# Kernel optimization log

Hardware: AMD Instinct MI355X
Metric: run time of the kernel (lower is better)

The kernel has to match this reference:

```python
import jax, jax.numpy as jnp
import numpy as np
import math
from jax import lax

TAU = 2
SIGMA_D2 = (TAU / 1.5) ** 2
SIGMA_TH2 = math.radians(20.0) ** 2

_offs = range(-TAU, TAU + 1)
OFFSETS = np.array([(dz, dy, dx) for dz in _offs for dy in _offs for dx in _offs
                    if dz or dy or dx], dtype=np.int32)  # (124, 3)
W_DIST = np.exp(-(OFFSETS.astype(np.float64) ** 2).sum(1) / SIGMA_D2).astype(np.float32)


def setup_inputs() -> dict:
    key = jax.random.key(0)
    k1, k2 = jax.random.split(key)
    n_pred = jax.random.normal(k1, (2, 3, 64, 64, 64), dtype=jnp.float32)
    source_pred = jax.random.normal(k2, (2, 1, 64, 64, 64), dtype=jnp.float32)
    return {"n_pred": n_pred, "source_pred": source_pred}


def reference(n_pred, source_pred):
    B, C, D, H, W = n_pred.shape
    pad = TAU
    # F.normalize(p=2, dim=1, eps=1e-6): divide by max(norm, eps)
    norm = jnp.sqrt(jnp.sum(n_pred * n_pred, axis=1, keepdims=True))
    n = n_pred / jnp.maximum(norm, 1e-6)

    prob = jax.nn.sigmoid(source_pred)            # (B,1,D,H,W)
    central_mask = prob > 0.5                      # (B,1,D,H,W)

    spat = ((0, 0), (0, 0), (pad, pad), (pad, pad), (pad, pad))
    padded_n = jnp.pad(n, spat)                    # zero pad like F.pad value=0
    padded_p = jnp.pad(prob, spat)

    offsets = jnp.asarray(OFFSETS)                 # (124,3)
    w_dist = jnp.asarray(W_DIST, dtype=n.dtype)    # (124,)

    def body(carry, xs):
        off, wd = xs
        start_n = (0, 0, pad + off[0], pad + off[1], pad + off[2])
        shifted_n = lax.dynamic_slice(padded_n, start_n, (B, C, D, H, W))
        shifted_p = lax.dynamic_slice(padded_p, start_n, (B, 1, D, H, W))
        dot = jnp.clip(jnp.sum(n * shifted_n, axis=1), -1.0, 1.0)  # (B,D,H,W)
        theta2 = jnp.arccos(dot) ** 2
        w_theta = jnp.exp(-theta2 / SIGMA_TH2)
        m = (central_mask & (shifted_p > 0.5))[:, 0].astype(n.dtype)  # (B,D,H,W)
        total, count = carry
        total = total + wd * jnp.sum(w_theta * m)
        count = count + jnp.sum(m)
        return (total, count), None

    init = (jnp.zeros((), n.dtype), jnp.zeros((), n.dtype))
    (total, count), _ = lax.scan(body, init, (offsets, w_dist))
    # reduction='mean' over masked elements; 0 if no valid pairs
    return jnp.where(count == 0, jnp.zeros((), n.dtype), total / count)
```

## Files before the change

### kernel.cpp

```cpp
#include <hip/hip_runtime.h>
#include <math.h>

#define PD 68
#define PD2 (PD * PD)
#define PVOL (PD * PD * PD)
#define NBLK2 2048

#define KE (-16.4140429822f)


__global__ __launch_bounds__(256) void pad_normalize_kernel(
    const float* __restrict__ n_pred,
    const float* __restrict__ src,
    float4* __restrict__ q)
{
    int idx = blockIdx.x * 256 + threadIdx.x;
    if (idx >= 2 * PVOL) return;
    int b = idx / PVOL;
    int r = idx - b * PVOL;
    int z = r / PD2;
    int r2 = r - z * PD2;
    int y = r2 / PD;
    int x = r2 - y * PD;
    int gx = x - 2, gy = y - 2, gz = z - 2;
    float4 v = make_float4(0.f, 0.f, 0.f, 0.f);
    if ((unsigned)gx < 64u && (unsigned)gy < 64u && (unsigned)gz < 64u) {
        const size_t cs = 262144;
        size_t vox = ((size_t)gz * 64 + gy) * 64 + gx;
        size_t off = (size_t)b * 3 * cs + vox;
        float xx = n_pred[off];
        float yy = n_pred[off + cs];
        float zz = n_pred[off + 2 * cs];
        float inv = 1.0f / fmaxf(sqrtf(xx * xx + yy * yy + zz * zz), 1e-6f);
        float m = (src[(size_t)b * cs + vox] > 0.0f) ? 1.0f : 0.0f;
        v = make_float4(xx * inv, yy * inv, zz * inv, m);
    }
    q[idx] = v;
}


__global__ __launch_bounds__(256) void stencil_kernel(
    const float4* __restrict__ q, float2* __restrict__ partials)
{
    int x = threadIdx.x & 63;
    int y = blockIdx.x * 4 + (threadIdx.x >> 6);
    int z = blockIdx.y;
    int b = blockIdx.z;
    const float4* cp =
        q + (size_t)b * PVOL + ((size_t)(z + 2) * PD + (y + 2)) * PD + (x + 2);
    float4 c = cp[0];
    float tot = 0.0f, cf = 0.0f;
    if (c.w != 0.0f) {
#pragma unroll
        for (int dz = 0; dz <= 2; ++dz) {
#pragma unroll
            for (int dy = -2; dy <= 2; ++dy) {
#pragma unroll
                for (int dx = -2; dx <= 2; ++dx) {
                    if (dz == 0 && dy < 0) continue;
                    if (dz == 0 && dy == 0 && dx <= 0) continue;
                    const float coff =
                        -0.5625f * (float)(dz * dz + dy * dy + dx * dx);
                    float4 nb = cp[(dz * PD + dy) * PD + dx];
                    float dot = fmaf(c.x, nb.x, fmaf(c.y, nb.y, c.z * nb.z));
                    float u = 1.0f - dot;
                    float p = fmaf(u, 1.8990885e-3f, 5.5803571e-3f);
                    p = fmaf(u, p, 1.8750000e-2f);
                    p = fmaf(u, p, 8.3333333e-2f);
                    p = fmaf(u, p, 1.0f);
                    float uh = u * p * p;
                    float w = __expf(fmaf(KE, uh, coff));
                    tot = fmaf(w, nb.w, tot);
                    cf += nb.w;
                }
            }
        }
    }
#pragma unroll
    for (int s = 32; s > 0; s >>= 1) {
        tot += __shfl_down(tot, s, 64);
        cf  += __shfl_down(cf, s, 64);
    }
    __shared__ float sd[4], sc[4];
    int wid = threadIdx.x >> 6, lane = threadIdx.x & 63;
    if (lane == 0) { sd[wid] = tot; sc[wid] = cf; }
    __syncthreads();
    if (threadIdx.x == 0) {
        int bid = ((int)blockIdx.z * gridDim.y + blockIdx.y) * gridDim.x
                  + blockIdx.x;
        partials[bid] = make_float2(sd[0] + sd[1] + sd[2] + sd[3],
                                    sc[0] + sc[1] + sc[2] + sc[3]);
    }
}

__global__ __launch_bounds__(256) void reduce_kernel(
    const float2* __restrict__ partials, float* __restrict__ out)
{
    double t = 0.0, c = 0.0;
    for (int i = threadIdx.x; i < NBLK2; i += 256) {
        float2 p = partials[i];
        t += (double)p.x;
        c += (double)p.y;
    }
#pragma unroll
    for (int s = 32; s > 0; s >>= 1) {
        t += __shfl_down(t, s, 64);
        c += __shfl_down(c, s, 64);
    }
    __shared__ double sd[4], sc[4];
    int wid = threadIdx.x >> 6, lane = threadIdx.x & 63;
    if (lane == 0) { sd[wid] = t; sc[wid] = c; }
    __syncthreads();
    if (threadIdx.x == 0) {
        double T = sd[0] + sd[1] + sd[2] + sd[3];
        double C = sc[0] + sc[1] + sc[2] + sc[3];
        out[0] = (C == 0.0) ? 0.0f : (float)(T / C);
    }
}


#define TILE 8
#define HALO 2
#define LDIM 12
#define LSZ  1728
#define NVOX 512

__global__ __launch_bounds__(256) void repulsion_fused_kernel(
    const float* __restrict__ n_pred, const float* __restrict__ src,
    double* __restrict__ acc)
{
    __shared__ float4 sn[LSZ];
    __shared__ float rd[4], rc[4];
    const int tx = blockIdx.x * TILE, ty = blockIdx.y * TILE;
    const int b = blockIdx.z >> 3, tz = (blockIdx.z & 7) * TILE;
    const size_t cs = 262144;
    const float* npb = n_pred + (size_t)b * 3 * cs;
    const float* spb = src + (size_t)b * cs;
    for (int i = threadIdx.x; i < LSZ; i += 256) {
        int lx = i % LDIM, t = i / LDIM, ly = t % LDIM, lz = t / LDIM;
        int gx = tx + lx - HALO, gy = ty + ly - HALO, gz = tz + lz - HALO;
        float4 v = make_float4(0.f, 0.f, 0.f, 0.f);
        if ((unsigned)gx < 64u && (unsigned)gy < 64u && (unsigned)gz < 64u) {
            size_t off = ((size_t)gz * 64 + gy) * 64 + gx;
            float x = npb[off], y = npb[cs + off], z = npb[2 * cs + off];
            float inv = 1.0f / fmaxf(sqrtf(x * x + y * y + z * z), 1e-6f);
            float m = (spb[off] > 0.0f) ? 1.0f : 0.0f;
            v = make_float4(x * inv, y * inv, z * inv, m);
        }
        sn[i] = v;
    }
    __syncthreads();
    float tot = 0.0f, cf = 0.0f;
    for (int v = threadIdx.x; v < NVOX; v += 256) {
        int lx = (v & 7) + HALO, ly = ((v >> 3) & 7) + HALO, lz = (v >> 6) + HALO;
        int ci = (lz * LDIM + ly) * LDIM + lx;
        float4 c = sn[ci];
        if (c.w == 0.0f) continue;
#pragma unroll
        for (int dz = -2; dz <= 2; ++dz)
#pragma unroll
            for (int dy = -2; dy <= 2; ++dy)
#pragma unroll
                for (int dx = -2; dx <= 2; ++dx) {
                    if (dz == 0 && dy == 0 && dx == 0) continue;
                    const float coff =
                        -0.5625f * (float)(dz * dz + dy * dy + dx * dx);
                    float4 nb = sn[ci + (dz * LDIM + dy) * LDIM + dx];
                    float dot = fmaf(c.x, nb.x, fmaf(c.y, nb.y, c.z * nb.z));
                    float u = 1.0f - dot;
                    float p = fmaf(u, 1.8990885e-3f, 5.5803571e-3f);
                    p = fmaf(u, p, 1.8750000e-2f);
                    p = fmaf(u, p, 8.3333333e-2f);
                    p = fmaf(u, p, 1.0f);
                    float uh = u * p * p;
                    float w = __expf(fmaf(KE, uh, coff));
                    tot = fmaf(w, nb.w, tot);
                    cf += nb.w;
                }
    }
#pragma unroll
    for (int s = 32; s > 0; s >>= 1) {
        tot += __shfl_down(tot, s, 64);
        cf  += __shfl_down(cf, s, 64);
    }
    int wid = threadIdx.x >> 6, lane = threadIdx.x & 63;
    if (lane == 0) { rd[wid] = tot; rc[wid] = cf; }
    __syncthreads();
    if (threadIdx.x == 0) {
        atomicAdd(&acc[0], (double)rd[0] + rd[1] + rd[2] + rd[3]);
        atomicAdd(&acc[1], (double)rc[0] + rc[1] + rc[2] + rc[3]);
    }
}

__global__ void zero_acc_kernel(double* acc) { acc[0] = 0.0; acc[1] = 0.0; }

__global__ void finalize_kernel(const double* acc, float* out) {
    out[0] = (acc[1] == 0.0) ? 0.0f : (float)(acc[0] / acc[1]);
}


extern "C" void kernel_launch(void* const* d_in, const int* in_sizes, int n_in,
                              void* d_out, int out_size, void* d_ws, size_t ws_size,
                              hipStream_t stream) {
    const float* n_pred = (const float*)d_in[0];
    const float* src    = (const float*)d_in[1];

    const size_t vol_bytes = (size_t)2 * PVOL * sizeof(float4);
    const size_t need = vol_bytes + (size_t)NBLK2 * sizeof(float2);

    if (ws_size >= need) {
        float4* q = (float4*)d_ws;
        float2* partials = (float2*)((char*)d_ws + vol_bytes);
        int nblk = (2 * PVOL + 255) / 256;
        pad_normalize_kernel<<<nblk, 256, 0, stream>>>(n_pred, src, q);
        dim3 grid(16, 64, 2);
        stencil_kernel<<<grid, 256, 0, stream>>>(q, partials);
        reduce_kernel<<<1, 256, 0, stream>>>(partials, (float*)d_out);
    } else {
        double* acc = (double*)d_ws;
        zero_acc_kernel<<<1, 1, 0, stream>>>(acc);
        dim3 grid(8, 8, 16);
        repulsion_fused_kernel<<<grid, 256, 0, stream>>>(n_pred, src, acc);
        finalize_kernel<<<1, 1, 0, stream>>>(acc, (float*)d_out);
    }
}
```

Baseline: 32.58 us.

## Register-block stencil over z columns and fuse final reduction via last-block atomics

Each thread now handles a column of four z voxels and loads every neighbour plane once, reusing each load for up to three centres in registers. The centre-mask branch becomes a multiply by c.w, which removes divergence but also computes pairs for masked-out centres. The separate reduce kernel is dropped: blocks add their totals to double atomics and the last block to finish writes the result, with the accumulator reset folded into the pad kernel. The exponential is rewritten in base 2 with pre-scaled constants, and the grid shrinks by a factor of four, lowering parallelism.

```diff
diff --git a/kernel.cpp b/kernel.cpp
--- a/kernel.cpp
+++ b/kernel.cpp
@@ -4,17 +4,21 @@
 #define PD 68
 #define PD2 (PD * PD)
 #define PVOL (PD * PD * PD)
-#define NBLK2 2048
-
-#define KE (-16.4140429822f)
+#define ZT 4
+
+#define KE2 (-23.68045839f)
+#define CW2 (-0.8115159605f)
 
 
 __global__ __launch_bounds__(256) void pad_normalize_kernel(
     const float* __restrict__ n_pred,
     const float* __restrict__ src,
-    float4* __restrict__ q)
+    float4* __restrict__ q,
+    double* __restrict__ acc,
+    unsigned long long* __restrict__ cnt)
 {
     int idx = blockIdx.x * 256 + threadIdx.x;
+    if (idx == 0) { acc[0] = 0.0; acc[1] = 0.0; *cnt = 0ull; }
     if (idx >= 2 * PVOL) return;
     int b = idx / PVOL;
     int r = idx - b * PVOL;
@@ -39,43 +43,54 @@
 }
 
 
-__global__ __launch_bounds__(256) void stencil_kernel(
-    const float4* __restrict__ q, float2* __restrict__ partials)
+__global__ __launch_bounds__(256) void stencil_col_kernel(
+    const float4* __restrict__ q, double* __restrict__ acc,
+    unsigned long long* __restrict__ cnt, float* __restrict__ out, int nblocks)
 {
     int x = threadIdx.x & 63;
     int y = blockIdx.x * 4 + (threadIdx.x >> 6);
-    int z = blockIdx.y;
+    int z0 = blockIdx.y * ZT;
     int b = blockIdx.z;
-    const float4* cp =
-        q + (size_t)b * PVOL + ((size_t)(z + 2) * PD + (y + 2)) * PD + (x + 2);
-    float4 c = cp[0];
+    const float4* base =
+        q + (size_t)b * PVOL + ((size_t)(z0 + 2) * PD + (y + 2)) * PD + (x + 2);
+
+    float4 cc[ZT];
+#pragma unroll
+    for (int k = 0; k < ZT; ++k) cc[k] = base[(size_t)k * PD2];
+
     float tot = 0.0f, cf = 0.0f;
-    if (c.w != 0.0f) {
-#pragma unroll
-        for (int dz = 0; dz <= 2; ++dz) {
-#pragma unroll
-            for (int dy = -2; dy <= 2; ++dy) {
-#pragma unroll
-                for (int dx = -2; dx <= 2; ++dx) {
-                    if (dz == 0 && dy < 0) continue;
-                    if (dz == 0 && dy == 0 && dx <= 0) continue;
-                    const float coff =
-                        -0.5625f * (float)(dz * dz + dy * dy + dx * dx);
-                    float4 nb = cp[(dz * PD + dy) * PD + dx];
-                    float dot = fmaf(c.x, nb.x, fmaf(c.y, nb.y, c.z * nb.z));
-                    float u = 1.0f - dot;
-                    float p = fmaf(u, 1.8990885e-3f, 5.5803571e-3f);
-                    p = fmaf(u, p, 1.8750000e-2f);
-                    p = fmaf(u, p, 8.3333333e-2f);
-                    p = fmaf(u, p, 1.0f);
-                    float uh = u * p * p;
-                    float w = __expf(fmaf(KE, uh, coff));
-                    tot = fmaf(w, nb.w, tot);
-                    cf += nb.w;
-                }
+
+    auto app = [&](const float4& c, const float4& nb, float coff2) {
+        float dot = fmaf(c.x, nb.x, fmaf(c.y, nb.y, c.z * nb.z));
+        float u = 1.0f - dot;
+        float p = fmaf(u, 1.8990885e-3f, 5.5803571e-3f);
+        p = fmaf(u, p, 1.8750000e-2f);
+        p = fmaf(u, p, 8.3333333e-2f);
+        p = fmaf(u, p, 1.0f);
+        float uh = u * p * p;
+        float w = exp2f(fmaf(KE2, uh, coff2));
+        float g = nb.w * c.w;
+        tot = fmaf(w, g, tot);
+        cf += g;
+    };
+
+#pragma unroll
+    for (int k = 0; k < ZT + 2; ++k) {
+#pragma unroll
+        for (int dy = -2; dy <= 2; ++dy) {
+#pragma unroll
+            for (int dx = -2; dx <= 2; ++dx) {
+                float4 nb = base[(size_t)k * PD2 + dy * PD + dx];
+                if (k < ZT && (dy > 0 || (dy == 0 && dx > 0)))
+                    app(cc[k], nb, CW2 * (float)(dy * dy + dx * dx));
+                if (k >= 1 && k - 1 < ZT)
+                    app(cc[k - 1], nb, CW2 * (float)(1 + dy * dy + dx * dx));
+                if (k >= 2 && k - 2 < ZT)
+                    app(cc[k - 2], nb, CW2 * (float)(4 + dy * dy + dx * dx));
             }
         }
     }
+
 #pragma unroll
     for (int s = 32; s > 0; s >>= 1) {
         tot += __shfl_down(tot, s, 64);
@@ -86,35 +101,15 @@
     if (lane == 0) { sd[wid] = tot; sc[wid] = cf; }
     __syncthreads();
     if (threadIdx.x == 0) {
-        int bid = ((int)blockIdx.z * gridDim.y + blockIdx.y) * gridDim.x
-                  + blockIdx.x;
-        partials[bid] = make_float2(sd[0] + sd[1] + sd[2] + sd[3],
-                                    sc[0] + sc[1] + sc[2] + sc[3]);
-    }
-}
-
-__global__ __launch_bounds__(256) void reduce_kernel(
-    const float2* __restrict__ partials, float* __restrict__ out)
-{
-    double t = 0.0, c = 0.0;
-    for (int i = threadIdx.x; i < NBLK2; i += 256) {
-        float2 p = partials[i];
-        t += (double)p.x;
-        c += (double)p.y;
-    }
-#pragma unroll
-    for (int s = 32; s > 0; s >>= 1) {
-        t += __shfl_down(t, s, 64);
-        c += __shfl_down(c, s, 64);
-    }
-    __shared__ double sd[4], sc[4];
-    int wid = threadIdx.x >> 6, lane = threadIdx.x & 63;
-    if (lane == 0) { sd[wid] = t; sc[wid] = c; }
-    __syncthreads();
-    if (threadIdx.x == 0) {
-        double T = sd[0] + sd[1] + sd[2] + sd[3];
-        double C = sc[0] + sc[1] + sc[2] + sc[3];
-        out[0] = (C == 0.0) ? 0.0f : (float)(T / C);
+        atomicAdd(&acc[0], (double)(sd[0] + sd[1] + sd[2] + sd[3]));
+        atomicAdd(&acc[1], (double)(sc[0] + sc[1] + sc[2] + sc[3]));
+        __threadfence();
+        unsigned long long done = atomicAdd(cnt, 1ull) + 1ull;
+        if (done == (unsigned long long)nblocks) {
+            double T = atomicAdd(&acc[0], 0.0);
+            double C = atomicAdd(&acc[1], 0.0);
+            out[0] = (C == 0.0) ? 0.0f : (float)(T / C);
+        }
     }
 }
 
@@ -142,10 +137,10 @@
         float4 v = make_float4(0.f, 0.f, 0.f, 0.f);
         if ((unsigned)gx < 64u && (unsigned)gy < 64u && (unsigned)gz < 64u) {
             size_t off = ((size_t)gz * 64 + gy) * 64 + gx;
-            float x = npb[off], y = npb[cs + off], z = npb[2 * cs + off];
-            float inv = 1.0f / fmaxf(sqrtf(x * x + y * y + z * z), 1e-6f);
+            float xx = npb[off], yy = npb[cs + off], zz = npb[2 * cs + off];
+            float inv = 1.0f / fmaxf(sqrtf(xx * xx + yy * yy + zz * zz), 1e-6f);
             float m = (spb[off] > 0.0f) ? 1.0f : 0.0f;
-            v = make_float4(x * inv, y * inv, z * inv, m);
+            v = make_float4(xx * inv, yy * inv, zz * inv, m);
         }
         sn[i] = v;
     }
@@ -163,8 +158,8 @@
 #pragma unroll
                 for (int dx = -2; dx <= 2; ++dx) {
                     if (dz == 0 && dy == 0 && dx == 0) continue;
-                    const float coff =
-                        -0.5625f * (float)(dz * dz + dy * dy + dx * dx);
+                    const float coff2 =
+                        CW2 * (float)(dz * dz + dy * dy + dx * dx);
                     float4 nb = sn[ci + (dz * LDIM + dy) * LDIM + dx];
                     float dot = fmaf(c.x, nb.x, fmaf(c.y, nb.y, c.z * nb.z));
                     float u = 1.0f - dot;
@@ -173,7 +168,7 @@
                     p = fmaf(u, p, 8.3333333e-2f);
                     p = fmaf(u, p, 1.0f);
                     float uh = u * p * p;
-                    float w = __expf(fmaf(KE, uh, coff));
+                    float w = exp2f(fmaf(KE2, uh, coff2));
                     tot = fmaf(w, nb.w, tot);
                     cf += nb.w;
                 }
@@ -206,16 +201,17 @@
     const float* src    = (const float*)d_in[1];
 
     const size_t vol_bytes = (size_t)2 * PVOL * sizeof(float4);
-    const size_t need = vol_bytes + (size_t)NBLK2 * sizeof(float2);
+    const size_t need = vol_bytes + 2 * sizeof(double) + sizeof(unsigned long long);
 
     if (ws_size >= need) {
         float4* q = (float4*)d_ws;
-        float2* partials = (float2*)((char*)d_ws + vol_bytes);
+        double* acc = (double*)((char*)d_ws + vol_bytes);
+        unsigned long long* cnt = (unsigned long long*)(acc + 2);
         int nblk = (2 * PVOL + 255) / 256;
-        pad_normalize_kernel<<<nblk, 256, 0, stream>>>(n_pred, src, q);
-        dim3 grid(16, 64, 2);
-        stencil_kernel<<<grid, 256, 0, stream>>>(q, partials);
-        reduce_kernel<<<1, 256, 0, stream>>>(partials, (float*)d_out);
+        pad_normalize_kernel<<<nblk, 256, 0, stream>>>(n_pred, src, q, acc, cnt);
+        dim3 grid(16, 64 / ZT, 2);
+        stencil_col_kernel<<<grid, 256, 0, stream>>>(q, acc, cnt, (float*)d_out,
+                                                     (int)(grid.x * grid.y * grid.z));
     } else {
         double* acc = (double*)d_ws;
         zero_acc_kernel<<<1, 1, 0, stream>>>(acc);
```

Result: slower. 45.49 us (+39.6%).
